# Kernel tuning notes

Hardware: AMD Instinct MI355X
Metric: run time of the kernel (lower is better)

Reference implementation:

```python
import jax, jax.numpy as jnp
import numpy as np

WS = 7
NUM_HEADS = 12
DIM = 384
HEAD_DIM = DIM // NUM_HEADS
SCALE = HEAD_DIM ** -0.5


def _rel_pos_index(ws: int) -> jnp.ndarray:
    coords = np.stack(np.meshgrid(np.arange(ws), np.arange(ws), indexing='ij'))  # (2, ws, ws)
    cf = coords.reshape(2, -1)                       # (2, ws*ws)
    rel = cf[:, :, None] - cf[:, None, :]            # (2, N, N)
    rel = rel.transpose(1, 2, 0).copy()              # (N, N, 2)
    rel[..., 0] += ws - 1
    rel[..., 1] += ws - 1
    rel[..., 0] *= 2 * ws - 1
    return jnp.asarray(rel.sum(-1))                  # (N, N) int indices into bias table


REL_IDX = _rel_pos_index(WS)


def setup_inputs() -> dict:
    key = jax.random.key(0)
    ks = jax.random.split(key, 7)
    BW, N, C = 4096, WS * WS, DIM
    num_win = 64
    return {
        'x': jax.random.normal(ks[0], (BW, N, C), jnp.float32),
        'mask': jax.random.normal(ks[1], (num_win, N, N), jnp.float32),
        'qkv_w': jax.random.normal(ks[2], (3 * C, C), jnp.float32) * 0.02,
        'qkv_b': jax.random.normal(ks[3], (3 * C,), jnp.float32) * 0.02,
        'proj_w': jax.random.normal(ks[4], (C, C), jnp.float32) * 0.02,
        'proj_b': jax.random.normal(ks[5], (C,), jnp.float32) * 0.02,
        'bias_table': jax.random.normal(ks[6], ((2 * WS - 1) ** 2, NUM_HEADS), jnp.float32) * 0.02,
    }


def reference(x, mask, qkv_w, qkv_b, proj_w, proj_b, bias_table):
    BW, N, C = x.shape
    H, hd = NUM_HEADS, HEAD_DIM
    # QKV projection: (BW, N, 3C) -> (3, BW, H, N, hd)
    qkv = (x @ qkv_w.T + qkv_b).reshape(BW, N, 3, H, hd).transpose(2, 0, 3, 1, 4)
    q, k, v = qkv[0], qkv[1], qkv[2]
    attn = jnp.einsum('bhnd,bhmd->bhnm', q, k) * SCALE  # (BW, H, N, N)
    bias = bias_table[REL_IDX]                          # (N, N, H)
    attn = attn + bias.transpose(2, 0, 1)[None]
    num_win = mask.shape[0]
    attn = attn.reshape(BW // num_win, num_win, H, N, N) + mask[None, :, None]
    attn = attn.reshape(BW, H, N, N)
    attn = jax.nn.softmax(attn, axis=-1)
    out = jnp.einsum('bhnm,bhmd->bhnd', attn, v)        # (BW, H, N, hd)
    out = out.transpose(0, 2, 1, 3).reshape(BW, N, C)
    return out @ proj_w.T + proj_b
```

## Files before the change

kernel.cpp:

```cpp
#include <hip/hip_runtime.h>

typedef unsigned short u16;
typedef unsigned int u32;
typedef __attribute__((ext_vector_type(8))) short short8;
typedef __attribute__((ext_vector_type(4))) float floatx4;

#define SCALE_Q 0.17677669529663687f

__device__ __forceinline__ u16 f2bf(float f) {
  u32 u = __float_as_uint(f);
  u = (u + 0x7fffu + ((u >> 16) & 1u)) >> 16;
  return (u16)u;
}

__device__ __forceinline__ void gload_lds16(const void* g, void* l) {
  __builtin_amdgcn_global_load_lds(
      (const __attribute__((address_space(1))) u32*)g,
      (__attribute__((address_space(3))) u32*)l, 16, 0, 0);
}

__device__ __forceinline__ floatx4 mfma16(short8 a, short8 b, floatx4 c) {
  return __builtin_amdgcn_mfma_f32_16x16x32_bf16(a, b, c, 0, 0, 0);
}

__global__ void cast_w_kernel(const float* __restrict__ qkv_w,
                              const float* __restrict__ proj_w,
                              u16* __restrict__ wb1, u16* __restrict__ wb2) {
  int idx = blockIdx.x * 256 + threadIdx.x;
  wb1[idx] = f2bf(qkv_w[idx]);
  if (idx < 147456) wb2[idx] = f2bf(proj_w[idx]);
}

__global__ __launch_bounds__(256) void cast_x_kernel(const float* __restrict__ x,
                                                     u16* __restrict__ xb) {
  const size_t i = ((size_t)blockIdx.x * 256 + threadIdx.x) * 8;
  const float4 f0 = *(const float4*)(x + i);
  const float4 f1 = *(const float4*)(x + i + 4);
  uint4 pk;
  pk.x = (u32)f2bf(f0.x) | ((u32)f2bf(f0.y) << 16);
  pk.y = (u32)f2bf(f0.z) | ((u32)f2bf(f0.w) << 16);
  pk.z = (u32)f2bf(f1.x) | ((u32)f2bf(f1.y) << 16);
  pk.w = (u32)f2bf(f1.z) | ((u32)f2bf(f1.w) << 16);
  *(uint4*)(xb + i) = pk;
}

__global__ void comb_kernel(const float* __restrict__ bias_table,
                            const float* __restrict__ mask,
                            float* __restrict__ comb) {
  int wh = blockIdx.x;
  int w = wh / 12, h = wh - w * 12;
  float* dst = comb + (size_t)wh * 4096;
  for (int e = threadIdx.x; e < 4096; e += 256) {
    int q = e >> 6, p = e & 63;
    float v;
    if (q >= 49) v = -1e30f;
    else if (p >= 49) v = 0.0f;
    else {
      int pi = p / 7, pj = p - pi * 7;
      int qi = q / 7, qj = q - qi * 7;
      int ridx = (pi - qi + 6) * 13 + (pj - qj + 6);
      v = bias_table[ridx * 12 + h] + mask[(size_t)w * 2401 + p * 49 + q];
    }
    dst[e] = v;
  }
}

__global__ __launch_bounds__(256) void qkv_gemm(const u16* __restrict__ A,
                                                const u16* __restrict__ B,
                                                const float* __restrict__ bias,
                                                u16* __restrict__ C) {
  __shared__ u16 As[128 * 32];
  __shared__ u16 Bs[128 * 32];
  const int tid = threadIdx.x;
  const int lane = tid & 63;
  const int wave = tid >> 6;
  const int l15 = lane & 15;
  const int quad = lane >> 4;
  const int wr = wave >> 1, wc = wave & 1;
  const u32 bid = blockIdx.x;
  const u32 xcd = bid & 7;
  const u32 slot = bid >> 3;
  const u32 grp = slot / 9;
  const u32 tn = slot - grp * 9;
  const u32 tm = xcd * 196 + grp;

  floatx4 acc[4][4];
#pragma unroll
  for (int i = 0; i < 4; ++i)
#pragma unroll
    for (int j = 0; j < 4; ++j) acc[i][j] = (floatx4){0.f, 0.f, 0.f, 0.f};

  for (int kb = 0; kb < 12; ++kb) {
    const int k0 = kb * 32;
#pragma unroll
    for (int r = 0; r < 2; ++r) {
      const int c = r * 256 + tid;
      const int m = c >> 2, kp = c & 3;
      gload_lds16(A + (size_t)(tm * 128 + m) * 384 + k0 + kp * 8, &As[c * 8]);
      gload_lds16(B + (size_t)(tn * 128 + m) * 384 + k0 + kp * 8, &Bs[c * 8]);
    }
    __syncthreads();
    short8 af[4], bfr[4];
#pragma unroll
    for (int i = 0; i < 4; ++i)
      af[i] = *(const short8*)(&As[(wr * 64 + i * 16 + l15) * 32 + quad * 8]);
#pragma unroll
    for (int i = 0; i < 4; ++i)
      bfr[i] = *(const short8*)(&Bs[(wc * 64 + i * 16 + l15) * 32 + quad * 8]);
#pragma unroll
    for (int mi = 0; mi < 4; ++mi)
#pragma unroll
      for (int ni = 0; ni < 4; ++ni)
        acc[mi][ni] = mfma16(af[mi], bfr[ni], acc[mi][ni]);
    __syncthreads();
  }
  const float scale = (tn < 3) ? SCALE_Q : 1.0f;
#pragma unroll
  for (int ni = 0; ni < 4; ++ni) {
    const int gcol = tn * 128 + wc * 64 + ni * 16 + l15;
    const float bb = bias[gcol];
#pragma unroll
    for (int mi = 0; mi < 4; ++mi) {
      const int grow0 = tm * 128 + wr * 64 + mi * 16 + quad * 4;
#pragma unroll
      for (int r = 0; r < 4; ++r)
        C[(size_t)(grow0 + r) * 1152 + gcol] = f2bf((acc[mi][ni][r] + bb) * scale);
    }
  }
}

__global__ __launch_bounds__(64) void attn_kernel(const u16* __restrict__ qkv,
                                                  const float* __restrict__ comb,
                                                  u16* __restrict__ ao) {
  __shared__ uint4 smem4[864];
  u16* Ps = (u16*)smem4;
  u16* Vt = (u16*)((char*)smem4 + 9216);

  const int tid = threadIdx.x;
  const int l15 = tid & 15, quad = tid >> 4;
  const int bh = blockIdx.x;
  const int b = bh / 12, h = bh - b * 12;
  const int w = b & 63;

  const uint4 z = make_uint4(0u, 0u, 0u, 0u);
  for (int i = tid; i < 288; i += 64) smem4[576 + i] = z;

  const size_t base = (size_t)b * 49 * 1152 + (size_t)h * 32;
  const u16* vbase = qkv + base + 768;
  for (int s0 = tid; s0 < 196; s0 += 64) {
    const int t = s0 >> 2, part = s0 & 3;
    const uint4 dv = *(const uint4*)(vbase + (size_t)t * 1152 + part * 8);
    const int d0 = part * 8;
    const u32 vv[4] = {dv.x, dv.y, dv.z, dv.w};
#pragma unroll
    for (int j = 0; j < 4; ++j) {
      Vt[(d0 + 2 * j) * 72 + t] = (u16)(vv[j] & 0xffffu);
      Vt[(d0 + 2 * j + 1) * 72 + t] = (u16)(vv[j] >> 16);
    }
  }

  const u16* qbase = qkv + base + quad * 8;
  short8 aq[4], bk[4];
  const short8 z8 = {0, 0, 0, 0, 0, 0, 0, 0};
#pragma unroll
  for (int i = 0; i < 3; ++i) {
    aq[i] = *(const short8*)(qbase + (size_t)(i * 16 + l15) * 1152);
    bk[i] = *(const short8*)(qbase + 384 + (size_t)(i * 16 + l15) * 1152);
  }
  aq[3] = (l15 == 0) ? *(const short8*)(qbase + (size_t)48 * 1152) : z8;
  bk[3] = (l15 == 0) ? *(const short8*)(qbase + 384 + (size_t)48 * 1152) : z8;

  floatx4 s[4][4];
  const floatx4 z4 = (floatx4){0.f, 0.f, 0.f, 0.f};
#pragma unroll
  for (int mi = 0; mi < 4; ++mi)
#pragma unroll
    for (int ni = 0; ni < 4; ++ni) s[mi][ni] = mfma16(aq[mi], bk[ni], z4);

  const float* cb = comb + (size_t)(w * 12 + h) * 4096;
#pragma unroll
  for (int ni = 0; ni < 4; ++ni)
#pragma unroll
    for (int mi = 0; mi < 4; ++mi) {
      const float4 cv = *(const float4*)(cb + (ni * 16 + l15) * 64 + mi * 16 + quad * 4);
      s[mi][ni][0] += cv.x;
      s[mi][ni][1] += cv.y;
      s[mi][ni][2] += cv.z;
      s[mi][ni][3] += cv.w;
    }

  floatx4 mx[4], sm[4];
#pragma unroll
  for (int mi = 0; mi < 4; ++mi)
#pragma unroll
    for (int r = 0; r < 4; ++r)
      mx[mi][r] = fmaxf(fmaxf(s[mi][0][r], s[mi][1][r]), fmaxf(s[mi][2][r], s[mi][3][r]));
#pragma unroll
  for (int d = 1; d < 16; d <<= 1)
#pragma unroll
    for (int mi = 0; mi < 4; ++mi)
#pragma unroll
      for (int r = 0; r < 4; ++r)
        mx[mi][r] = fmaxf(mx[mi][r], __shfl_xor(mx[mi][r], d));
#pragma unroll
  for (int mi = 0; mi < 4; ++mi)
#pragma unroll
    for (int r = 0; r < 4; ++r) {
      float a = 0.f;
#pragma unroll
      for (int ni = 0; ni < 4; ++ni) {
        const float e = __expf(s[mi][ni][r] - mx[mi][r]);
        s[mi][ni][r] = e;
        a += e;
      }
      sm[mi][r] = a;
    }
#pragma unroll
  for (int d = 1; d < 16; d <<= 1)
#pragma unroll
    for (int mi = 0; mi < 4; ++mi)
#pragma unroll
      for (int r = 0; r < 4; ++r)
        sm[mi][r] += __shfl_xor(sm[mi][r], d);

#pragma unroll
  for (int mi = 0; mi < 4; ++mi)
#pragma unroll
    for (int r = 0; r < 4; ++r) {
      const float rinv = 1.0f / sm[mi][r];
      const int row = mi * 16 + quad * 4 + r;
#pragma unroll
      for (int ni = 0; ni < 4; ++ni)
        Ps[row * 72 + ni * 16 + l15] = f2bf(s[mi][ni][r] * rinv);
    }
  __syncthreads();

  floatx4 o[4][2];
#pragma unroll
  for (int mi = 0; mi < 4; ++mi)
#pragma unroll
    for (int ni = 0; ni < 2; ++ni) o[mi][ni] = z4;
#pragma unroll
  for (int kk = 0; kk < 2; ++kk) {
    short8 ap[4], bv[2];
#pragma unroll
    for (int mi = 0; mi < 4; ++mi)
      ap[mi] = *(const short8*)(Ps + (mi * 16 + l15) * 72 + kk * 32 + quad * 8);
#pragma unroll
    for (int ni = 0; ni < 2; ++ni)
      bv[ni] = *(const short8*)(Vt + (ni * 16 + l15) * 72 + kk * 32 + quad * 8);
#pragma unroll
    for (int mi = 0; mi < 4; ++mi)
#pragma unroll
      for (int ni = 0; ni < 2; ++ni) o[mi][ni] = mfma16(ap[mi], bv[ni], o[mi][ni]);
  }
#pragma unroll
  for (int mi = 0; mi < 4; ++mi)
#pragma unroll
    for (int r = 0; r < 4; ++r) {
      const int row = mi * 16 + quad * 4 + r;
      if (row < 49) {
        u16* dst = ao + (size_t)(b * 49 + row) * 384 + h * 32;
#pragma unroll
        for (int ni = 0; ni < 2; ++ni)
          dst[ni * 16 + l15] = f2bf(o[mi][ni][r]);
      }
    }
}

__global__ __launch_bounds__(256) void proj_gemm(const u16* __restrict__ A,
                                                 const u16* __restrict__ B,
                                                 const float* __restrict__ bias,
                                                 float* __restrict__ C) {
  __shared__ u16 As[128 * 32];
  __shared__ u16 Bs[128 * 32];
  const int tid = threadIdx.x;
  const int lane = tid & 63;
  const int wave = tid >> 6;
  const int l15 = lane & 15;
  const int quad = lane >> 4;
  const int wr = wave >> 1, wc = wave & 1;
  const u32 bid = blockIdx.x;
  const u32 xcd = bid & 7;
  const u32 slot = bid >> 3;
  const u32 grp = slot / 3;
  const u32 tn = slot - grp * 3;
  const u32 tm = xcd * 196 + grp;

  floatx4 acc[4][4];
#pragma unroll
  for (int i = 0; i < 4; ++i)
#pragma unroll
    for (int j = 0; j < 4; ++j) acc[i][j] = (floatx4){0.f, 0.f, 0.f, 0.f};

  for (int kb = 0; kb < 12; ++kb) {
    const int k0 = kb * 32;
#pragma unroll
    for (int r = 0; r < 2; ++r) {
      const int c = r * 256 + tid;
      const int m = c >> 2, kp = c & 3;
      gload_lds16(A + (size_t)(tm * 128 + m) * 384 + k0 + kp * 8, &As[c * 8]);
      gload_lds16(B + (size_t)(tn * 128 + m) * 384 + k0 + kp * 8, &Bs[c * 8]);
    }
    __syncthreads();
    short8 af[4], bfr[4];
#pragma unroll
    for (int i = 0; i < 4; ++i)
      af[i] = *(const short8*)(&As[(wr * 64 + i * 16 + l15) * 32 + quad * 8]);
#pragma unroll
    for (int i = 0; i < 4; ++i)
      bfr[i] = *(const short8*)(&Bs[(wc * 64 + i * 16 + l15) * 32 + quad * 8]);
#pragma unroll
    for (int mi = 0; mi < 4; ++mi)
#pragma unroll
      for (int ni = 0; ni < 4; ++ni)
        acc[mi][ni] = mfma16(af[mi], bfr[ni], acc[mi][ni]);
    __syncthreads();
  }
#pragma unroll
  for (int ni = 0; ni < 4; ++ni) {
    const int gcol = tn * 128 + wc * 64 + ni * 16 + l15;
    const float bb = bias[gcol];
#pragma unroll
    for (int mi = 0; mi < 4; ++mi) {
      const int grow0 = tm * 128 + wr * 64 + mi * 16 + quad * 4;
#pragma unroll
      for (int r = 0; r < 4; ++r)
        C[(size_t)(grow0 + r) * 384 + gcol] = acc[mi][ni][r] + bb;
    }
  }
}

extern "C" void kernel_launch(void* const* d_in, const int* in_sizes, int n_in,
                              void* d_out, int out_size, void* d_ws, size_t ws_size,
                              hipStream_t stream) {
  const float* x = (const float*)d_in[0];
  const float* mask = (const float*)d_in[1];
  const float* qkv_w = (const float*)d_in[2];
  const float* qkv_b = (const float*)d_in[3];
  const float* proj_w = (const float*)d_in[4];
  const float* proj_b = (const float*)d_in[5];
  const float* bias_table = (const float*)d_in[6];
  float* out = (float*)d_out;
  char* ws = (char*)d_ws;

  u16* wb1 = (u16*)(ws);
  u16* wb2 = (u16*)(ws + 884736);
  float* comb = (float*)(ws + 1179648);
  u16* qkvb = (u16*)(ws + 13762560);
  u16* ao = (u16*)(ws + 476184576);
  u16* xb = ao;

  hipLaunchKernelGGL(cast_w_kernel, dim3(1728), dim3(256), 0, stream, qkv_w, proj_w, wb1, wb2);
  hipLaunchKernelGGL(cast_x_kernel, dim3(37632), dim3(256), 0, stream, x, xb);
  hipLaunchKernelGGL(comb_kernel, dim3(768), dim3(256), 0, stream, bias_table, mask, comb);
  hipLaunchKernelGGL(qkv_gemm, dim3(14112), dim3(256), 0, stream, xb, wb1, qkv_b, qkvb);
  hipLaunchKernelGGL(attn_kernel, dim3(49152), dim3(64), 0, stream, qkvb, comb, ao);
  hipLaunchKernelGGL(proj_gemm, dim3(4704), dim3(256), 0, stream, ao, wb2, proj_b, out);
}
```

Measured before the change: 1.210 ms.

## Double-buffer GEMM LDS tiles and store QKV head-major for attention

```diff
diff --git a/kernel.cpp b/kernel.cpp
--- a/kernel.cpp
+++ b/kernel.cpp
@@ -69,8 +69,8 @@
                                                 const u16* __restrict__ B,
                                                 const float* __restrict__ bias,
                                                 u16* __restrict__ C) {
-  __shared__ u16 As[128 * 32];
-  __shared__ u16 Bs[128 * 32];
+  __shared__ u16 As[2][4096];
+  __shared__ u16 Bs[2][4096];
   const int tid = threadIdx.x;
   const int lane = tid & 63;
   const int wave = tid >> 6;
@@ -84,47 +84,72 @@
   const u32 tn = slot - grp * 9;
   const u32 tm = xcd * 196 + grp;
 
+  const int kp0 = tid >> 7, mm = tid & 127;
+  const u16* Ab0 = A + (size_t)tm * 49152 + mm * 384 + kp0 * 8;
+  const u16* Ab1 = Ab0 + 2 * 8;
+  const u16* Bb0 = B + (size_t)tn * 49152 + mm * 384 + kp0 * 8;
+  const u16* Bb1 = Bb0 + 2 * 8;
+  const int ld0 = tid * 8, ld1 = ld0 + 2048;
+
   floatx4 acc[4][4];
 #pragma unroll
   for (int i = 0; i < 4; ++i)
 #pragma unroll
     for (int j = 0; j < 4; ++j) acc[i][j] = (floatx4){0.f, 0.f, 0.f, 0.f};
 
+#define QSTAGE(buf, k0)                       \
+  do {                                        \
+    gload_lds16(Ab0 + (k0), &As[buf][ld0]);   \
+    gload_lds16(Ab1 + (k0), &As[buf][ld1]);   \
+    gload_lds16(Bb0 + (k0), &Bs[buf][ld0]);   \
+    gload_lds16(Bb1 + (k0), &Bs[buf][ld1]);   \
+  } while (0)
+
+  QSTAGE(0, 0);
+  __syncthreads();
+
+  const int abase = (wr * 64 + l15) * 8 + quad * 1024;
+  const int bbase = (wc * 64 + l15) * 8 + quad * 1024;
+#pragma unroll
   for (int kb = 0; kb < 12; ++kb) {
-    const int k0 = kb * 32;
-#pragma unroll
-    for (int r = 0; r < 2; ++r) {
-      const int c = r * 256 + tid;
-      const int m = c >> 2, kp = c & 3;
-      gload_lds16(A + (size_t)(tm * 128 + m) * 384 + k0 + kp * 8, &As[c * 8]);
-      gload_lds16(B + (size_t)(tn * 128 + m) * 384 + k0 + kp * 8, &Bs[c * 8]);
-    }
-    __syncthreads();
+    const int cur = kb & 1;
+    if (kb < 11) QSTAGE(cur ^ 1, (kb + 1) * 32);
     short8 af[4], bfr[4];
 #pragma unroll
     for (int i = 0; i < 4; ++i)
-      af[i] = *(const short8*)(&As[(wr * 64 + i * 16 + l15) * 32 + quad * 8]);
+      af[i] = *(const short8*)(&As[cur][abase + i * 128]);
 #pragma unroll
     for (int i = 0; i < 4; ++i)
-      bfr[i] = *(const short8*)(&Bs[(wc * 64 + i * 16 + l15) * 32 + quad * 8]);
+      bfr[i] = *(const short8*)(&Bs[cur][bbase + i * 128]);
 #pragma unroll
     for (int mi = 0; mi < 4; ++mi)
 #pragma unroll
       for (int ni = 0; ni < 4; ++ni)
         acc[mi][ni] = mfma16(af[mi], bfr[ni], acc[mi][ni]);
-    __syncthreads();
-  }
-  const float scale = (tn < 3) ? SCALE_Q : 1.0f;
+    if (kb < 11) __syncthreads();
+  }
+#undef QSTAGE
+
 #pragma unroll
   for (int ni = 0; ni < 4; ++ni) {
-    const int gcol = tn * 128 + wc * 64 + ni * 16 + l15;
-    const float bb = bias[gcol];
+    const int gbase = (int)tn * 128 + wc * 64 + ni * 16;
+    const int which = gbase / 384;
+    const int rem = gbase - which * 384;
+    const int h = rem >> 5;
+    const int db = rem & 31;
+    const float bb = bias[gbase + l15];
+    const float scale = (which == 0) ? SCALE_Q : 1.0f;
+    u16* hp = C + ((size_t)which * 49152 + h) * 1568 + db + l15;
 #pragma unroll
     for (int mi = 0; mi < 4; ++mi) {
-      const int grow0 = tm * 128 + wr * 64 + mi * 16 + quad * 4;
-#pragma unroll
-      for (int r = 0; r < 4; ++r)
-        C[(size_t)(grow0 + r) * 1152 + gcol] = f2bf((acc[mi][ni][r] + bb) * scale);
+      const int grow0 = (int)tm * 128 + wr * 64 + mi * 16 + quad * 4;
+#pragma unroll
+      for (int r = 0; r < 4; ++r) {
+        const int grow = grow0 + r;
+        const int b = grow / 49;
+        const int tok = grow - b * 49;
+        hp[(size_t)b * 18816 + tok * 32] = f2bf((acc[mi][ni][r] + bb) * scale);
+      }
     }
   }
 }
@@ -142,14 +167,27 @@
   const int b = bh / 12, h = bh - b * 12;
   const int w = b & 63;
 
+  const size_t hoff = (size_t)bh * 1568;
+  const u16* qb = qkv + hoff;
+  const u16* kbp = qkv + (size_t)49152 * 1568 + hoff;
+  const u16* vb = qkv + (size_t)98304 * 1568 + hoff;
+
+  short8 aq[4], bk[4];
+  const short8 z8 = {0, 0, 0, 0, 0, 0, 0, 0};
+#pragma unroll
+  for (int i = 0; i < 3; ++i) {
+    aq[i] = *(const short8*)(qb + (i * 16 + l15) * 32 + quad * 8);
+    bk[i] = *(const short8*)(kbp + (i * 16 + l15) * 32 + quad * 8);
+  }
+  aq[3] = (l15 == 0) ? *(const short8*)(qb + 48 * 32 + quad * 8) : z8;
+  bk[3] = (l15 == 0) ? *(const short8*)(kbp + 48 * 32 + quad * 8) : z8;
+
   const uint4 z = make_uint4(0u, 0u, 0u, 0u);
   for (int i = tid; i < 288; i += 64) smem4[576 + i] = z;
 
-  const size_t base = (size_t)b * 49 * 1152 + (size_t)h * 32;
-  const u16* vbase = qkv + base + 768;
   for (int s0 = tid; s0 < 196; s0 += 64) {
     const int t = s0 >> 2, part = s0 & 3;
-    const uint4 dv = *(const uint4*)(vbase + (size_t)t * 1152 + part * 8);
+    const uint4 dv = *(const uint4*)(vb + t * 32 + part * 8);
     const int d0 = part * 8;
     const u32 vv[4] = {dv.x, dv.y, dv.z, dv.w};
 #pragma unroll
@@ -159,23 +197,14 @@
     }
   }
 
-  const u16* qbase = qkv + base + quad * 8;
-  short8 aq[4], bk[4];
-  const short8 z8 = {0, 0, 0, 0, 0, 0, 0, 0};
-#pragma unroll
-  for (int i = 0; i < 3; ++i) {
-    aq[i] = *(const short8*)(qbase + (size_t)(i * 16 + l15) * 1152);
-    bk[i] = *(const short8*)(qbase + 384 + (size_t)(i * 16 + l15) * 1152);
-  }
-  aq[3] = (l15 == 0) ? *(const short8*)(qbase + (size_t)48 * 1152) : z8;
-  bk[3] = (l15 == 0) ? *(const short8*)(qbase + 384 + (size_t)48 * 1152) : z8;
-
   floatx4 s[4][4];
   const floatx4 z4 = (floatx4){0.f, 0.f, 0.f, 0.f};
+  __builtin_amdgcn_s_setprio(1);
 #pragma unroll
   for (int mi = 0; mi < 4; ++mi)
 #pragma unroll
     for (int ni = 0; ni < 4; ++ni) s[mi][ni] = mfma16(aq[mi], bk[ni], z4);
+  __builtin_amdgcn_s_setprio(0);
 
   const float* cb = comb + (size_t)(w * 12 + h) * 4096;
 #pragma unroll
@@ -249,10 +278,12 @@
 #pragma unroll
     for (int ni = 0; ni < 2; ++ni)
       bv[ni] = *(const short8*)(Vt + (ni * 16 + l15) * 72 + kk * 32 + quad * 8);
+    __builtin_amdgcn_s_setprio(1);
 #pragma unroll
     for (int mi = 0; mi < 4; ++mi)
 #pragma unroll
       for (int ni = 0; ni < 2; ++ni) o[mi][ni] = mfma16(ap[mi], bv[ni], o[mi][ni]);
+    __builtin_amdgcn_s_setprio(0);
   }
 #pragma unroll
   for (int mi = 0; mi < 4; ++mi)
@@ -272,8 +303,8 @@
                                                  const u16* __restrict__ B,
                                                  const float* __restrict__ bias,
                                                  float* __restrict__ C) {
-  __shared__ u16 As[128 * 32];
-  __shared__ u16 Bs[128 * 32];
+  __shared__ u16 As[2][4096];
+  __shared__ u16 Bs[2][4096];
   const int tid = threadIdx.x;
   const int lane = tid & 63;
   const int wave = tid >> 6;
@@ -287,36 +318,52 @@
   const u32 tn = slot - grp * 3;
   const u32 tm = xcd * 196 + grp;
 
+  const int kp0 = tid >> 7, mm = tid & 127;
+  const u16* Ab0 = A + (size_t)tm * 49152 + mm * 384 + kp0 * 8;
+  const u16* Ab1 = Ab0 + 2 * 8;
+  const u16* Bb0 = B + (size_t)tn * 49152 + mm * 384 + kp0 * 8;
+  const u16* Bb1 = Bb0 + 2 * 8;
+  const int ld0 = tid * 8, ld1 = ld0 + 2048;
+
   floatx4 acc[4][4];
 #pragma unroll
   for (int i = 0; i < 4; ++i)
 #pragma unroll
     for (int j = 0; j < 4; ++j) acc[i][j] = (floatx4){0.f, 0.f, 0.f, 0.f};
 
+#define PSTAGE(buf, k0)                       \
+  do {                                        \
+    gload_lds16(Ab0 + (k0), &As[buf][ld0]);   \
+    gload_lds16(Ab1 + (k0), &As[buf][ld1]);   \
+    gload_lds16(Bb0 + (k0), &Bs[buf][ld0]);   \
+    gload_lds16(Bb1 + (k0), &Bs[buf][ld1]);   \
+  } while (0)
+
+  PSTAGE(0, 0);
+  __syncthreads();
+
+  const int abase = (wr * 64 + l15) * 8 + quad * 1024;
+  const int bbase = (wc * 64 + l15) * 8 + quad * 1024;
+#pragma unroll
   for (int kb = 0; kb < 12; ++kb) {
-    const int k0 = kb * 32;
-#pragma unroll
-    for (int r = 0; r < 2; ++r) {
-      const int c = r * 256 + tid;
-      const int m = c >> 2, kp = c & 3;
-      gload_lds16(A + (size_t)(tm * 128 + m) * 384 + k0 + kp * 8, &As[c * 8]);
-      gload_lds16(B + (size_t)(tn * 128 + m) * 384 + k0 + kp * 8, &Bs[c * 8]);
-    }
-    __syncthreads();
+    const int cur = kb & 1;
+    if (kb < 11) PSTAGE(cur ^ 1, (kb + 1) * 32);
     short8 af[4], bfr[4];
 #pragma unroll
     for (int i = 0; i < 4; ++i)
-      af[i] = *(const short8*)(&As[(wr * 64 + i * 16 + l15) * 32 + quad * 8]);
+      af[i] = *(const short8*)(&As[cur][abase + i * 128]);
 #pragma unroll
     for (int i = 0; i < 4; ++i)
-      bfr[i] = *(const short8*)(&Bs[(wc * 64 + i * 16 + l15) * 32 + quad * 8]);
+      bfr[i] = *(const short8*)(&Bs[cur][bbase + i * 128]);
 #pragma unroll
     for (int mi = 0; mi < 4; ++mi)
 #pragma unroll
       for (int ni = 0; ni < 4; ++ni)
         acc[mi][ni] = mfma16(af[mi], bfr[ni], acc[mi][ni]);
-    __syncthreads();
-  }
+    if (kb < 11) __syncthreads();
+  }
+#undef PSTAGE
+
 #pragma unroll
   for (int ni = 0; ni < 4; ++ni) {
     const int gcol = tn * 128 + wc * 64 + ni * 16 + l15;
```

Result: slower. 1.356 ms (+12.1%).
